# Kernel optimization log

Measured on AMD Instinct MI355X. Metric: run time of the kernel, lower is better.

Reference implementation:

```python
import jax, jax.numpy as jnp
import numpy as np


def _gcn_layer(x, row, col, W, b):
    # x: [N, d_in]; row/col: [E'] (with self loops already appended)
    N = x.shape[0]
    deg = jax.ops.segment_sum(jnp.ones_like(row, dtype=x.dtype), row, num_segments=N)
    deg_inv_sqrt = deg ** -0.5  # self loops guarantee deg >= 1
    norm = deg_inv_sqrt[row] * deg_inv_sqrt[col]  # [E']
    msg = norm[:, None] * x[row]                  # gather + normalize
    aggr = jax.ops.segment_sum(msg, col, num_segments=N)  # scatter-add
    return aggr @ W + b


def reference(x, edge_index, W1, b1, W2, b2):
    N = x.shape[0]
    loops = jnp.arange(N, dtype=edge_index.dtype)
    row = jnp.concatenate([edge_index[0], loops])
    col = jnp.concatenate([edge_index[1], loops])
    h = jax.nn.relu(_gcn_layer(x, row, col, W1, b1))
    # F.dropout(training=self.training) is identity in eval mode
    out = _gcn_layer(h, row, col, W2, b2)
    return jax.nn.log_softmax(out, axis=1)


def setup_inputs() -> dict:
    key = jax.random.key(0)
    k1, k2, k3, k4 = jax.random.split(key, 4)
    N, E, F_IN, F_HID, F_OUT = 100000, 1200000, 64, 64, 16
    x = jax.random.normal(k1, (N, F_IN), dtype=jnp.float32)
    edge_index = jax.random.randint(k2, (2, E), 0, N, dtype=jnp.int64)
    W1 = jax.random.normal(k3, (F_IN, F_HID), dtype=jnp.float32) / np.sqrt(F_IN)
    b1 = jnp.zeros((F_HID,), dtype=jnp.float32)
    W2 = jax.random.normal(k4, (F_HID, F_OUT), dtype=jnp.float32) / np.sqrt(F_HID)
    b2 = jnp.zeros((F_OUT,), dtype=jnp.float32)
    return {"x": x, "edge_index": edge_index, "W1": W1, "b1": b1, "W2": W2, "b2": b2}
```

## Files before the change

### kernel.cpp

```cpp
#include <hip/hip_runtime.h>
#include <hip/hip_bf16.h>

typedef __attribute__((ext_vector_type(8))) _Float16 hfrag;
typedef __attribute__((ext_vector_type(4))) float ffrag;
typedef __attribute__((ext_vector_type(4))) _Float16 h4v;

#define BSH 8
#define LBS 256
#define CAP_SH 14
#define CAP (1 << CAP_SH)
#define CONV_BLKS 384
#define FILL_BLKS 512

__device__ __forceinline__ float b2f_(unsigned short u) {
    return __uint_as_float(((unsigned)u) << 16);
}
__device__ __forceinline__ unsigned short f2b_(float v) {
    __hip_bfloat16 h = __float2bfloat16(v);
    return *reinterpret_cast<unsigned short*>(&h);
}
__device__ __forceinline__ unsigned short f2h_(float v) {
    _Float16 h = (_Float16)v;
    return __builtin_bit_cast(unsigned short, h);
}
__device__ __forceinline__ float h2f_(unsigned short u) {
    _Float16 h = __builtin_bit_cast(_Float16, u);
    return (float)h;
}

__device__ __forceinline__ float loadF(const void* p, long long i, int isF32) {
    if (isF32) return ((const float*)p)[i];
    return b2f_(((const unsigned short*)p)[i]);
}

__device__ __forceinline__ float4 loadF4(const void* p, long long base, int i4, int isF32) {
    if (isF32) {
        return ((const float4*)((const float*)p + base))[i4];
    } else {
        ushort4 u = ((const ushort4*)((const unsigned short*)p + base))[i4];
        return make_float4(b2f_(u.x), b2f_(u.y), b2f_(u.z), b2f_(u.w));
    }
}

__device__ __forceinline__ void get_edge(const int* ei, int i64, int e, int E, int& s, int& d) {
    if (i64) { s = ei[2 * (long long)e]; d = ei[2 * (long long)E + 2 * (long long)e]; }
    else     { s = ei[e];                d = ei[(long long)E + e]; }
}

struct E4 { int s[4]; int d[4]; };
__device__ __forceinline__ E4 load4(const int* __restrict__ ei, int i64, int e0, int E) {
    E4 r;
    if (i64) {
        const int4* ps = (const int4*)(ei + 2 * (long long)e0);
        const int4* pd = (const int4*)(ei + 2 * (long long)E + 2 * (long long)e0);
        int4 a = ps[0], b = ps[1];
        int4 c = pd[0], d = pd[1];
        r.s[0] = a.x; r.s[1] = a.z; r.s[2] = b.x; r.s[3] = b.z;
        r.d[0] = c.x; r.d[1] = c.z; r.d[2] = d.x; r.d[3] = d.z;
    } else {
        int4 a = *(const int4*)(ei + e0);
        int4 c = *(const int4*)(ei + (long long)E + e0);
        r.s[0] = a.x; r.s[1] = a.y; r.s[2] = a.z; r.s[3] = a.w;
        r.d[0] = c.x; r.d[1] = c.y; r.d[2] = c.z; r.d[3] = c.w;
    }
    return r;
}

__device__ __forceinline__ void wave_scan_excl(int* a, int nEl, int lane) {
    int run = 0;
    for (int base = 0; base < nEl; base += 64) {
        int i = base + lane;
        int orig = (i < nEl) ? a[i] : 0;
        int v = orig;
#pragma unroll
        for (int off = 1; off < 64; off <<= 1) {
            int u = __shfl_up(v, off);
            if (lane >= off) v += u;
        }
        if (i < nEl) a[i] = v - orig + run;
        run += __shfl(v, 63);
    }
}

__global__ void k_prep(const void* x, const int* ei,
                       const void* W1, const void* b1, const void* W2, const void* b2,
                       int E, int nbk,
                       int* flags, float* Wbuf, int* cur_d, int* cur_s) {
    __shared__ int s_sane, s_zero;
    int tid = threadIdx.x;
    if (tid == 0) { s_sane = 0; s_zero = 0; }
    __syncthreads();
    const unsigned short* xu = (const unsigned short*)x;
    int sane = 0;
    for (int k = tid; k < 4096; k += 256) {
        float v = b2f_(xu[2 * k]);
        float a = fabsf(v);
        if (v == 0.0f || (a >= 9.3e-10f && a <= 1.1e9f)) sane++;
    }
    if (sane) atomicAdd(&s_sane, sane);
    int zero = 0;
    for (int k = tid; k < 1024; k += 256) if (ei[2 * k + 1] == 0) zero++;
    if (zero) atomicAdd(&s_zero, zero);
    __syncthreads();
    int f = (s_sane < 3000) ? 1 : 0;
    if (tid == 0) { flags[0] = f; flags[1] = (s_zero > 512) ? 1 : 0; }
    for (int i = tid; i < nbk; i += 256) { cur_d[i] = i << CAP_SH; cur_s[i] = i << CAP_SH; }
    for (int i = tid; i < 4096; i += 256) Wbuf[i] = loadF(W1, i, f);
    if (tid < 64) Wbuf[4096 + tid] = loadF(b1, tid, f);
    for (int i = tid; i < 1024; i += 256) Wbuf[4160 + i] = loadF(W2, i, f);
    if (tid < 16) Wbuf[5184 + tid] = loadF(b2, tid, f);
}

__global__ __launch_bounds__(256) void k_stage(const void* __restrict__ x,
                                               const int* __restrict__ ei,
                                               const int* __restrict__ flags,
                                               int E, int N, int nbk,
                                               int* __restrict__ cur_d, int* __restrict__ cur_s,
                                               int* __restrict__ pdst,
                                               unsigned char* __restrict__ psrc,
                                               unsigned short* __restrict__ xh) {
    __shared__ int hd[512], hs[512], bd[512], bs[512];
    int tid = threadIdx.x;
    if (blockIdx.x < CONV_BLKS) {
        int f = flags[0];
        int n4 = N * 16;
        int ctid = blockIdx.x * 256 + tid;
        int stride = CONV_BLKS * 256 * 2;
        for (int i0 = ctid * 2; i0 < n4; i0 += stride) {
            float4 v0 = loadF4(x, 0, i0, f);
            float4 v1 = (i0 + 1 < n4) ? loadF4(x, 0, i0 + 1, f) : make_float4(0, 0, 0, 0);
            ushort4 o0, o1;
            o0.x = f2h_(v0.x); o0.y = f2h_(v0.y); o0.z = f2h_(v0.z); o0.w = f2h_(v0.w);
            o1.x = f2h_(v1.x); o1.y = f2h_(v1.y); o1.z = f2h_(v1.z); o1.w = f2h_(v1.w);
            ((ushort4*)xh)[i0] = o0;
            if (i0 + 1 < n4) ((ushort4*)xh)[i0 + 1] = o1;
        }
        return;
    }
    for (int i = tid; i < 512; i += 256) { hd[i] = 0; hs[i] = 0; }
    __syncthreads();
    int i64 = flags[1];
    int fb = blockIdx.x - CONV_BLKS;
    int ctid = fb * 256 + tid;
    int stride = FILL_BLKS * 256 * 8;
    for (int e0 = ctid * 8; e0 + 8 <= E; e0 += stride) {
        E4 a = load4(ei, i64, e0, E);
        E4 b = load4(ei, i64, e0 + 4, E);
#pragma unroll
        for (int u = 0; u < 4; ++u) {
            atomicAdd(&hd[a.d[u] >> BSH], 1);
            atomicAdd(&hs[a.s[u] >> BSH], 1);
            atomicAdd(&hd[b.d[u] >> BSH], 1);
            atomicAdd(&hs[b.s[u] >> BSH], 1);
        }
    }
    if (fb == 0 && tid == 0) {
        for (int e = E & ~7; e < E; ++e) {
            int s, d;
            get_edge(ei, i64, e, E, s, d);
            atomicAdd(&hd[d >> BSH], 1);
            atomicAdd(&hs[s >> BSH], 1);
        }
    }
    __syncthreads();
    for (int i = tid; i < nbk; i += 256) {
        int v = hd[i];
        bd[i] = v ? atomicAdd(&cur_d[i], v) : 0;
        v = hs[i];
        bs[i] = v ? atomicAdd(&cur_s[i], v) : 0;
    }
    __syncthreads();
    for (int e0 = ctid * 8; e0 + 8 <= E; e0 += stride) {
        E4 a = load4(ei, i64, e0, E);
        E4 b = load4(ei, i64, e0 + 4, E);
#pragma unroll
        for (int u = 0; u < 4; ++u) {
            int db = a.d[u] >> BSH, sb = a.s[u] >> BSH;
            int p = atomicAdd(&bd[db], 1);
            if (p < ((db + 1) << CAP_SH)) pdst[p] = (a.s[u] << BSH) | (a.d[u] & (LBS - 1));
            int q = atomicAdd(&bs[sb], 1);
            if (q < ((sb + 1) << CAP_SH)) psrc[q] = (unsigned char)(a.s[u] & (LBS - 1));
            db = b.d[u] >> BSH; sb = b.s[u] >> BSH;
            p = atomicAdd(&bd[db], 1);
            if (p < ((db + 1) << CAP_SH)) pdst[p] = (b.s[u] << BSH) | (b.d[u] & (LBS - 1));
            q = atomicAdd(&bs[sb], 1);
            if (q < ((sb + 1) << CAP_SH)) psrc[q] = (unsigned char)(b.s[u] & (LBS - 1));
        }
    }
    if (fb == 0 && tid == 0) {
        for (int e = E & ~7; e < E; ++e) {
            int s, d;
            get_edge(ei, i64, e, E, s, d);
            int db = d >> BSH, sb = s >> BSH;
            int p = atomicAdd(&bd[db], 1);
            if (p < ((db + 1) << CAP_SH)) pdst[p] = (s << BSH) | (d & (LBS - 1));
            int q = atomicAdd(&bs[sb], 1);
            if (q < ((sb + 1) << CAP_SH)) psrc[q] = (unsigned char)(s & (LBS - 1));
        }
    }
}

__global__ __launch_bounds__(256) void k_deg(const unsigned char* __restrict__ psrc,
                                             const int* __restrict__ cur_s,
                                             float* __restrict__ dis, int N) {
    __shared__ int h[LBS];
    int b = blockIdx.x, tid = threadIdx.x;
    if (tid < LBS) h[tid] = 0;
    __syncthreads();
    int beg = b << CAP_SH;
    int end = min(cur_s[b], (b + 1) << CAP_SH);
    int cnt = end - beg;
    int nv = cnt & ~3;
    for (int off = 4 * tid; off < nv; off += 1024) {
        uchar4 v = *(const uchar4*)(psrc + beg + off);
        atomicAdd(&h[v.x], 1); atomicAdd(&h[v.y], 1);
        atomicAdd(&h[v.z], 1); atomicAdd(&h[v.w], 1);
    }
    if (tid < cnt - nv) atomicAdd(&h[psrc[beg + nv + tid]], 1);
    __syncthreads();
    if (tid < LBS) {
        int node = b * LBS + tid;
        if (node < N) dis[node] = rsqrtf((float)h[tid] + 1.0f);
    }
}

__global__ __launch_bounds__(256) void k_csr(const int* __restrict__ pdst,
                                             const int* __restrict__ cur_d,
                                             const float* __restrict__ dis,
                                             int2* __restrict__ row_se,
                                             int2* __restrict__ pke, int N) {
    __shared__ int h[LBS], lb[LBS], cur[LBS];
    int b = blockIdx.x, tid = threadIdx.x;
    if (tid < LBS) h[tid] = 0;
    __syncthreads();
    int beg = b << CAP_SH;
    int end = min(cur_d[b], (b + 1) << CAP_SH);
    for (int p = beg + tid; p < end; p += 256) atomicAdd(&h[pdst[p] & (LBS - 1)], 1);
    __syncthreads();
    if (tid < LBS) lb[tid] = h[tid];
    __syncthreads();
    if (tid < 64) wave_scan_excl(lb, LBS, tid);
    __syncthreads();
    if (tid < LBS) {
        cur[tid] = lb[tid];
        int node = b * LBS + tid;
        if (node < N) row_se[node] = make_int2(beg + lb[tid], beg + lb[tid] + h[tid]);
    }
    __syncthreads();
    for (int p = beg + tid; p < end; p += 256) {
        int e = pdst[p];
        int src = e >> BSH, ld = e & (LBS - 1);
        int r = atomicAdd(&cur[ld], 1);
        pke[beg + r] = make_int2(src, __float_as_int(dis[src]));
    }
}

__global__ __launch_bounds__(256) void k_agg(const unsigned short* __restrict__ xh,
                                             const float* __restrict__ dis,
                                             const int2* __restrict__ row_se,
                                             const int2* __restrict__ pke,
                                             unsigned short* __restrict__ aggb, int N) {
    int tid = threadIdx.x;
    int lane = tid & 63;
    int g = lane >> 4, i4 = lane & 15;
    int n = blockIdx.x * 16 + (tid >> 6) * 4 + g;
    if (n >= N) return;
    float dd = dis[n];
    int2 se = row_se[n];
    int beg = se.x, end = se.y;
    int cnt = end - beg;
    h4v xv = *(const h4v*)(xh + (long long)n * 64 + i4 * 4);
    float w = dd * dd;
    float4 A[4];
    A[0].x = w * (float)xv[0]; A[0].y = w * (float)xv[1];
    A[0].z = w * (float)xv[2]; A[0].w = w * (float)xv[3];
#pragma unroll
    for (int u = 1; u < 4; ++u) A[u] = make_float4(0.f, 0.f, 0.f, 0.f);
    int T = (cnt + 3) >> 2;
    int p = beg;
    int2 e[4];
#pragma unroll
    for (int u = 0; u < 4; ++u) e[u] = pke[p + u];
    for (int t = 0; t < T; ++t) {
        h4v hv[4];
#pragma unroll
        for (int u = 0; u < 4; ++u) {
            unsigned ex = min((unsigned)e[u].x, (unsigned)(N - 1));
            hv[u] = *(const h4v*)(xh + (long long)ex * 64 + i4 * 4);
        }
        float nv[4];
#pragma unroll
        for (int u = 0; u < 4; ++u) nv[u] = (p + u < end) ? dd * __int_as_float(e[u].y) : 0.f;
#pragma unroll
        for (int u = 0; u < 4; ++u) e[u] = pke[p + 4 + u];
        p += 4;
#pragma unroll
        for (int u = 0; u < 4; ++u) {
            A[u].x += nv[u] * (float)hv[u][0];
            A[u].y += nv[u] * (float)hv[u][1];
            A[u].z += nv[u] * (float)hv[u][2];
            A[u].w += nv[u] * (float)hv[u][3];
        }
    }
    float4 s;
    s.x = A[0].x + A[1].x + A[2].x + A[3].x;
    s.y = A[0].y + A[1].y + A[2].y + A[3].y;
    s.z = A[0].z + A[1].z + A[2].z + A[3].z;
    s.w = A[0].w + A[1].w + A[2].w + A[3].w;
    ushort4 o;
    o.x = f2h_(s.x); o.y = f2h_(s.y); o.z = f2h_(s.z); o.w = f2h_(s.w);
    *(ushort4*)(aggb + (size_t)n * 64 + i4 * 4) = o;
}

__global__ __launch_bounds__(256) void k_dense(const unsigned short* __restrict__ aggb,
                                               const float* __restrict__ Wbuf,
                                               unsigned short* __restrict__ t2b, int N) {
    __shared__ __align__(16) unsigned short Hs[4][16 * 72];
    int tid = threadIdx.x;
    int lane = tid & 63;
    int w = tid >> 6;
    int m = lane & 15, q = lane >> 4;
    int n0 = blockIdx.x * 64 + w * 16;
    if (n0 >= N) return;

    hfrag Bw1[2][4];
#pragma unroll
    for (int kt = 0; kt < 2; ++kt)
#pragma unroll
        for (int nt = 0; nt < 4; ++nt)
#pragma unroll
            for (int j = 0; j < 8; ++j)
                Bw1[kt][nt][j] = (_Float16)Wbuf[(kt * 32 + q * 8 + j) * 64 + nt * 16 + m];
    hfrag Bw2[2];
#pragma unroll
    for (int kt = 0; kt < 2; ++kt)
#pragma unroll
        for (int j = 0; j < 8; ++j)
            Bw2[kt][j] = (_Float16)Wbuf[4160 + (kt * 32 + q * 8 + j) * 16 + m];
    float b1n[4];
#pragma unroll
    for (int nt = 0; nt < 4; ++nt) b1n[nt] = Wbuf[4096 + nt * 16 + m];

    const unsigned short* arow = aggb + (size_t)(n0 + m) * 64 + q * 8;
    hfrag A0 = *(const hfrag*)(arow);
    hfrag A1 = *(const hfrag*)(arow + 32);

    ffrag acc[4];
#pragma unroll
    for (int nt = 0; nt < 4; ++nt) {
        ffrag z = {0.f, 0.f, 0.f, 0.f};
        z = __builtin_amdgcn_mfma_f32_16x16x32_f16(A0, Bw1[0][nt], z, 0, 0, 0);
        z = __builtin_amdgcn_mfma_f32_16x16x32_f16(A1, Bw1[1][nt], z, 0, 0, 0);
        acc[nt] = z;
    }
    unsigned short* hs = &Hs[w][0];
#pragma unroll
    for (int nt = 0; nt < 4; ++nt)
#pragma unroll
        for (int r = 0; r < 4; ++r) {
            float hv = fmaxf(acc[nt][r] + b1n[nt], 0.0f);
            hs[(q * 4 + r) * 72 + nt * 16 + m] = f2h_(hv);
        }
    const unsigned short* hrow = hs + m * 72 + q * 8;
    hfrag H0 = *(const hfrag*)(hrow);
    hfrag H1 = *(const hfrag*)(hrow + 32);
    ffrag t2 = {0.f, 0.f, 0.f, 0.f};
    t2 = __builtin_amdgcn_mfma_f32_16x16x32_f16(H0, Bw2[0], t2, 0, 0, 0);
    t2 = __builtin_amdgcn_mfma_f32_16x16x32_f16(H1, Bw2[1], t2, 0, 0, 0);
#pragma unroll
    for (int r = 0; r < 4; ++r)
        t2b[(size_t)(n0 + q * 4 + r) * 16 + m] = f2h_(t2[r]);
}

__global__ __launch_bounds__(256) void k_l2(const unsigned short* __restrict__ t2b,
                                            const int* __restrict__ flags,
                                            const float* __restrict__ dis,
                                            const int2* __restrict__ row_se,
                                            const int2* __restrict__ pke,
                                            const float* __restrict__ Wbuf,
                                            void* __restrict__ out, int N) {
    int isF32 = flags[0];
    int tid = threadIdx.x, lane = tid & 63;
    int g = lane >> 4, i = lane & 15;
    int n = blockIdx.x * 16 + (tid >> 6) * 4 + g;
    if (n >= N) return;
    float dd = dis[n];
    int2 se = row_se[n];
    int beg = se.x, end = se.y;
    int cnt = end - beg;
    float A[4];
    A[0] = dd * dd * h2f_(t2b[(size_t)n * 16 + i]);
    A[1] = 0.f; A[2] = 0.f; A[3] = 0.f;
    int T = (cnt + 3) >> 2;
    int p = beg;
    int2 e[4];
#pragma unroll
    for (int u = 0; u < 4; ++u) e[u] = pke[p + u];
    for (int t = 0; t < T; ++t) {
        float r[4];
#pragma unroll
        for (int u = 0; u < 4; ++u) {
            unsigned ex = min((unsigned)e[u].x, (unsigned)(N - 1));
            r[u] = h2f_(t2b[(size_t)ex * 16 + i]);
        }
        float nv[4];
#pragma unroll
        for (int u = 0; u < 4; ++u) nv[u] = (p + u < end) ? dd * __int_as_float(e[u].y) : 0.f;
#pragma unroll
        for (int u = 0; u < 4; ++u) e[u] = pke[p + 4 + u];
        p += 4;
#pragma unroll
        for (int u = 0; u < 4; ++u) A[u] += nv[u] * r[u];
    }
    float a0 = A[0] + A[1] + A[2] + A[3];
    float v = a0 + Wbuf[5184 + i];
    float mx = v;
#pragma unroll
    for (int off = 8; off; off >>= 1) mx = fmaxf(mx, __shfl_xor(mx, off, 16));
    float ex = __expf(v - mx);
    float ss = ex;
#pragma unroll
    for (int off = 8; off; off >>= 1) ss += __shfl_xor(ss, off, 16);
    float r = v - mx - logf(ss);
    size_t oi = (size_t)n * 16 + i;
    if (isF32) ((float*)out)[oi] = r;
    else       ((unsigned short*)out)[oi] = f2b_(r);
}

extern "C" void kernel_launch(void* const* d_in, const int* in_sizes, int n_in,
                              void* d_out, int out_size, void* d_ws, size_t ws_size,
                              hipStream_t stream) {
    const void* x  = d_in[0];
    const int*  ei = (const int*)d_in[1];
    const void* W1 = d_in[2];
    const void* b1 = d_in[3];
    const void* W2 = d_in[4];
    const void* b2 = d_in[5];

    const int N = in_sizes[0] / 64;
    const int E = in_sizes[1] / 2;
    const int nbk = (N + LBS - 1) >> BSH;

    char* p = (char*)d_ws;
#define CARVE(ty, name, bytes) ty name = (ty)p; p += (((size_t)(bytes)) + 63) & ~(size_t)63;
    CARVE(int*,   flags,     16)
    CARVE(float*, Wbuf,      5200 * 4)
    CARVE(float*, dis,       (size_t)N * 4)
    CARVE(int2*,  row_se,    (size_t)N * 8)
    CARVE(int*,   cur_d,     (size_t)nbk * 4)
    CARVE(int*,   cur_s,     (size_t)nbk * 4)
    CARVE(int*,   pdst,      ((size_t)nbk << CAP_SH) * 4)
    CARVE(unsigned char*, psrc, ((size_t)nbk << CAP_SH))
    CARVE(int2*,  pke,       (((size_t)nbk << CAP_SH) + 64) * 8)
    CARVE(unsigned short*, xh,   (size_t)N * 64 * 2)
    CARVE(unsigned short*, aggb, (size_t)N * 64 * 2)
    CARVE(unsigned short*, t2b,  (size_t)N * 16 * 2)
#undef CARVE

    k_prep<<<1, 256, 0, stream>>>(x, ei, W1, b1, W2, b2, E, nbk, flags, Wbuf, cur_d, cur_s);
    k_stage<<<CONV_BLKS + FILL_BLKS, 256, 0, stream>>>(x, ei, flags, E, N, nbk,
                                                       cur_d, cur_s, pdst, psrc, xh);
    k_deg<<<nbk, 256, 0, stream>>>(psrc, cur_s, dis, N);
    k_csr<<<nbk, 256, 0, stream>>>(pdst, cur_d, dis, row_se, pke, N);
    k_agg<<<(N + 15) / 16, 256, 0, stream>>>(xh, dis, row_se, pke, aggb, N);
    k_dense<<<(N + 63) / 64, 256, 0, stream>>>(aggb, Wbuf, t2b, N);
    k_l2<<<(N + 15) / 16, 256, 0, stream>>>(t2b, flags, dis, row_se, pke, Wbuf, d_out, N);
}
```

Measured before the change: 202.1 us.

## Split edge bucketing into count, scan, fill kernels replacing global atomics

The fused histogram-and-fill stage is split into three kernels. The first writes per-block bucket counts, the second does a per-bucket exclusive scan across fill blocks, and the third scatters edges using deterministic per-block offsets. This removes global atomicAdd contention on bucket cursors and cuts the fill block count from 512 to 128. In exchange it adds two kernel launches, extra count and offset arrays, and a second pass over the edge list in a separate launch.

```diff
diff --git a/kernel.cpp b/kernel.cpp
--- a/kernel.cpp
+++ b/kernel.cpp
@@ -10,7 +10,8 @@
 #define CAP_SH 14
 #define CAP (1 << CAP_SH)
 #define CONV_BLKS 384
-#define FILL_BLKS 512
+#define NF 128
+#define NBKP 512
 
 __device__ __forceinline__ float b2f_(unsigned short u) {
     return __uint_as_float(((unsigned)u) << 16);
@@ -84,8 +85,7 @@
 
 __global__ void k_prep(const void* x, const int* ei,
                        const void* W1, const void* b1, const void* W2, const void* b2,
-                       int E, int nbk,
-                       int* flags, float* Wbuf, int* cur_d, int* cur_s) {
+                       int* flags, float* Wbuf) {
     __shared__ int s_sane, s_zero;
     int tid = threadIdx.x;
     if (tid == 0) { s_sane = 0; s_zero = 0; }
@@ -104,22 +104,19 @@
     __syncthreads();
     int f = (s_sane < 3000) ? 1 : 0;
     if (tid == 0) { flags[0] = f; flags[1] = (s_zero > 512) ? 1 : 0; }
-    for (int i = tid; i < nbk; i += 256) { cur_d[i] = i << CAP_SH; cur_s[i] = i << CAP_SH; }
     for (int i = tid; i < 4096; i += 256) Wbuf[i] = loadF(W1, i, f);
     if (tid < 64) Wbuf[4096 + tid] = loadF(b1, tid, f);
     for (int i = tid; i < 1024; i += 256) Wbuf[4160 + i] = loadF(W2, i, f);
     if (tid < 16) Wbuf[5184 + tid] = loadF(b2, tid, f);
 }
 
-__global__ __launch_bounds__(256) void k_stage(const void* __restrict__ x,
-                                               const int* __restrict__ ei,
-                                               const int* __restrict__ flags,
-                                               int E, int N, int nbk,
-                                               int* __restrict__ cur_d, int* __restrict__ cur_s,
-                                               int* __restrict__ pdst,
-                                               unsigned char* __restrict__ psrc,
-                                               unsigned short* __restrict__ xh) {
-    __shared__ int hd[512], hs[512], bd[512], bs[512];
+__global__ __launch_bounds__(256) void k_s1(const void* __restrict__ x,
+                                            const int* __restrict__ ei,
+                                            const int* __restrict__ flags,
+                                            int E, int N, int nbk,
+                                            int* __restrict__ cnt_d, int* __restrict__ cnt_s,
+                                            unsigned short* __restrict__ xh) {
+    __shared__ int hd[512], hs[512];
     int tid = threadIdx.x;
     if (blockIdx.x < CONV_BLKS) {
         int f = flags[0];
@@ -142,7 +139,7 @@
     int i64 = flags[1];
     int fb = blockIdx.x - CONV_BLKS;
     int ctid = fb * 256 + tid;
-    int stride = FILL_BLKS * 256 * 8;
+    int stride = NF * 256 * 8;
     for (int e0 = ctid * 8; e0 + 8 <= E; e0 += stride) {
         E4 a = load4(ei, i64, e0, E);
         E4 b = load4(ei, i64, e0 + 4, E);
@@ -164,12 +161,54 @@
     }
     __syncthreads();
     for (int i = tid; i < nbk; i += 256) {
-        int v = hd[i];
-        bd[i] = v ? atomicAdd(&cur_d[i], v) : 0;
-        v = hs[i];
-        bs[i] = v ? atomicAdd(&cur_s[i], v) : 0;
-    }
-    __syncthreads();
+        cnt_d[fb * NBKP + i] = hd[i];
+        cnt_s[fb * NBKP + i] = hs[i];
+    }
+}
+
+__global__ __launch_bounds__(128) void k_s2(const int* __restrict__ cnt_d,
+                                            const int* __restrict__ cnt_s,
+                                            int nbk,
+                                            int* __restrict__ base_d, int* __restrict__ base_s,
+                                            int* __restrict__ td, int* __restrict__ ts) {
+    __shared__ int vd[NF], vs[NF];
+    __shared__ int lastd, lasts;
+    int b = blockIdx.x, tid = threadIdx.x;
+    for (int i = tid; i < NF; i += 128) { vd[i] = cnt_d[i * NBKP + b]; vs[i] = cnt_s[i * NBKP + b]; }
+    __syncthreads();
+    if (tid == 0) lastd = vd[NF - 1];
+    if (tid == 1) lasts = vs[NF - 1];
+    __syncthreads();
+    int lane = tid & 63;
+    if (tid < 64)       wave_scan_excl(vd, NF, lane);
+    else if (tid < 128) wave_scan_excl(vs, NF, lane);
+    __syncthreads();
+    for (int i = tid; i < NF; i += 128) {
+        base_d[i * NBKP + b] = (b << CAP_SH) + vd[i];
+        base_s[i * NBKP + b] = (b << CAP_SH) + vs[i];
+    }
+    if (tid == 0) td[b] = (b << CAP_SH) + vd[NF - 1] + lastd;
+    if (tid == 1) ts[b] = (b << CAP_SH) + vs[NF - 1] + lasts;
+}
+
+__global__ __launch_bounds__(256) void k_fill(const int* __restrict__ ei,
+                                              const int* __restrict__ flags,
+                                              int E, int nbk,
+                                              const int* __restrict__ base_d,
+                                              const int* __restrict__ base_s,
+                                              int* __restrict__ pdst,
+                                              unsigned char* __restrict__ psrc) {
+    __shared__ int bd[512], bs[512];
+    int tid = threadIdx.x;
+    int fb = blockIdx.x;
+    for (int i = tid; i < nbk; i += 256) {
+        bd[i] = base_d[fb * NBKP + i];
+        bs[i] = base_s[fb * NBKP + i];
+    }
+    __syncthreads();
+    int i64 = flags[1];
+    int ctid = fb * 256 + tid;
+    int stride = NF * 256 * 8;
     for (int e0 = ctid * 8; e0 + 8 <= E; e0 += stride) {
         E4 a = load4(ei, i64, e0, E);
         E4 b = load4(ei, i64, e0 + 4, E);
@@ -201,14 +240,14 @@
 }
 
 __global__ __launch_bounds__(256) void k_deg(const unsigned char* __restrict__ psrc,
-                                             const int* __restrict__ cur_s,
+                                             const int* __restrict__ ts,
                                              float* __restrict__ dis, int N) {
     __shared__ int h[LBS];
     int b = blockIdx.x, tid = threadIdx.x;
     if (tid < LBS) h[tid] = 0;
     __syncthreads();
     int beg = b << CAP_SH;
-    int end = min(cur_s[b], (b + 1) << CAP_SH);
+    int end = min(ts[b], (b + 1) << CAP_SH);
     int cnt = end - beg;
     int nv = cnt & ~3;
     for (int off = 4 * tid; off < nv; off += 1024) {
@@ -225,7 +264,7 @@
 }
 
 __global__ __launch_bounds__(256) void k_csr(const int* __restrict__ pdst,
-                                             const int* __restrict__ cur_d,
+                                             const int* __restrict__ td,
                                              const float* __restrict__ dis,
                                              int2* __restrict__ row_se,
                                              int2* __restrict__ pke, int N) {
@@ -234,7 +273,7 @@
     if (tid < LBS) h[tid] = 0;
     __syncthreads();
     int beg = b << CAP_SH;
-    int end = min(cur_d[b], (b + 1) << CAP_SH);
+    int end = min(td[b], (b + 1) << CAP_SH);
     for (int p = beg + tid; p < end; p += 256) atomicAdd(&h[pdst[p] & (LBS - 1)], 1);
     __syncthreads();
     if (tid < LBS) lb[tid] = h[tid];
@@ -447,8 +486,12 @@
     CARVE(float*, Wbuf,      5200 * 4)
     CARVE(float*, dis,       (size_t)N * 4)
     CARVE(int2*,  row_se,    (size_t)N * 8)
-    CARVE(int*,   cur_d,     (size_t)nbk * 4)
-    CARVE(int*,   cur_s,     (size_t)nbk * 4)
+    CARVE(int*,   cnt_d,     (size_t)NF * NBKP * 4)
+    CARVE(int*,   cnt_s,     (size_t)NF * NBKP * 4)
+    CARVE(int*,   base_d,    (size_t)NF * NBKP * 4)
+    CARVE(int*,   base_s,    (size_t)NF * NBKP * 4)
+    CARVE(int*,   td,        (size_t)nbk * 4)
+    CARVE(int*,   ts,        (size_t)nbk * 4)
     CARVE(int*,   pdst,      ((size_t)nbk << CAP_SH) * 4)
     CARVE(unsigned char*, psrc, ((size_t)nbk << CAP_SH))
     CARVE(int2*,  pke,       (((size_t)nbk << CAP_SH) + 64) * 8)
@@ -457,11 +500,12 @@
     CARVE(unsigned short*, t2b,  (size_t)N * 16 * 2)
 #undef CARVE
 
-    k_prep<<<1, 256, 0, stream>>>(x, ei, W1, b1, W2, b2, E, nbk, flags, Wbuf, cur_d, cur_s);
-    k_stage<<<CONV_BLKS + FILL_BLKS, 256, 0, stream>>>(x, ei, flags, E, N, nbk,
-                                                       cur_d, cur_s, pdst, psrc, xh);
-    k_deg<<<nbk, 256, 0, stream>>>(psrc, cur_s, dis, N);
-    k_csr<<<nbk, 256, 0, stream>>>(pdst, cur_d, dis, row_se, pke, N);
+    k_prep<<<1, 256, 0, stream>>>(x, ei, W1, b1, W2, b2, flags, Wbuf);
+    k_s1<<<CONV_BLKS + NF, 256, 0, stream>>>(x, ei, flags, E, N, nbk, cnt_d, cnt_s, xh);
+    k_s2<<<nbk, 128, 0, stream>>>(cnt_d, cnt_s, nbk, base_d, base_s, td, ts);
+    k_fill<<<NF, 256, 0, stream>>>(ei, flags, E, nbk, base_d, base_s, pdst, psrc);
+    k_deg<<<nbk, 256, 0, stream>>>(psrc, ts, dis, N);
+    k_csr<<<nbk, 256, 0, stream>>>(pdst, td, dis, row_se, pke, N);
     k_agg<<<(N + 15) / 16, 256, 0, stream>>>(xh, dis, row_se, pke, aggb, N);
     k_dense<<<(N + 63) / 64, 256, 0, stream>>>(aggb, Wbuf, t2b, N);
     k_l2<<<(N + 15) / 16, 256, 0, stream>>>(t2b, flags, dis, row_se, pke, Wbuf, d_out, N);
```

New measurement: 217.0 us. 7.4% more time.

## Split bucket staging into histogram and deterministic fill kernels with global degree atomics

Applied to the files above, without the earlier changes.

Replaces the single-block prep plus fused histogram/fill kernel with a histogram kernel that writes per-block bucket counts into a transposed table and counts source degrees with global atomics. A separate fill kernel computes each block's bucket offsets by prefix-summing that table, then scatters destination-bucketed edges. The psrc staging array and the k_deg kernel are dropped, and dis is computed in the conversion blocks. The aim is to remove the global atomic offset reservation and the second source-bucket scatter. The cost is an extra edge-list read, a memset, and 100k-address global atomics for degree.

```diff
diff --git a/kernel.cpp b/kernel.cpp
--- a/kernel.cpp
+++ b/kernel.cpp
@@ -9,8 +9,8 @@
 #define LBS 256
 #define CAP_SH 14
 #define CAP (1 << CAP_SH)
+#define NF 192
 #define CONV_BLKS 384
-#define FILL_BLKS 512
 
 __device__ __forceinline__ float b2f_(unsigned short u) {
     return __uint_as_float(((unsigned)u) << 16);
@@ -82,49 +82,88 @@
     }
 }
 
-__global__ void k_prep(const void* x, const int* ei,
-                       const void* W1, const void* b1, const void* W2, const void* b2,
-                       int E, int nbk,
-                       int* flags, float* Wbuf, int* cur_d, int* cur_s) {
+__global__ __launch_bounds__(256) void k_h(const void* __restrict__ x,
+                                           const int* __restrict__ ei,
+                                           const void* __restrict__ W1, const void* __restrict__ b1,
+                                           const void* __restrict__ W2, const void* __restrict__ b2,
+                                           int E, int N, int nbk,
+                                           int* __restrict__ flags, float* __restrict__ Wbuf,
+                                           int* __restrict__ cnt_t, int* __restrict__ deg) {
+    __shared__ int hd[512];
     __shared__ int s_sane, s_zero;
     int tid = threadIdx.x;
     if (tid == 0) { s_sane = 0; s_zero = 0; }
     __syncthreads();
-    const unsigned short* xu = (const unsigned short*)x;
-    int sane = 0;
-    for (int k = tid; k < 4096; k += 256) {
-        float v = b2f_(xu[2 * k]);
-        float a = fabsf(v);
-        if (v == 0.0f || (a >= 9.3e-10f && a <= 1.1e9f)) sane++;
-    }
-    if (sane) atomicAdd(&s_sane, sane);
+    if (blockIdx.x == NF) {
+        const unsigned short* xu = (const unsigned short*)x;
+        int sane = 0;
+        for (int k = tid; k < 4096; k += 256) {
+            float v = b2f_(xu[2 * k]);
+            float a = fabsf(v);
+            if (v == 0.0f || (a >= 9.3e-10f && a <= 1.1e9f)) sane++;
+        }
+        if (sane) atomicAdd(&s_sane, sane);
+        int zero = 0;
+        for (int k = tid; k < 1024; k += 256) if (ei[2 * k + 1] == 0) zero++;
+        if (zero) atomicAdd(&s_zero, zero);
+        __syncthreads();
+        int f = (s_sane < 3000) ? 1 : 0;
+        if (tid == 0) { flags[0] = f; flags[1] = (s_zero > 512) ? 1 : 0; }
+        for (int i = tid; i < 4096; i += 256) Wbuf[i] = loadF(W1, i, f);
+        if (tid < 64) Wbuf[4096 + tid] = loadF(b1, tid, f);
+        for (int i = tid; i < 1024; i += 256) Wbuf[4160 + i] = loadF(W2, i, f);
+        if (tid < 16) Wbuf[5184 + tid] = loadF(b2, tid, f);
+        return;
+    }
     int zero = 0;
     for (int k = tid; k < 1024; k += 256) if (ei[2 * k + 1] == 0) zero++;
     if (zero) atomicAdd(&s_zero, zero);
-    __syncthreads();
-    int f = (s_sane < 3000) ? 1 : 0;
-    if (tid == 0) { flags[0] = f; flags[1] = (s_zero > 512) ? 1 : 0; }
-    for (int i = tid; i < nbk; i += 256) { cur_d[i] = i << CAP_SH; cur_s[i] = i << CAP_SH; }
-    for (int i = tid; i < 4096; i += 256) Wbuf[i] = loadF(W1, i, f);
-    if (tid < 64) Wbuf[4096 + tid] = loadF(b1, tid, f);
-    for (int i = tid; i < 1024; i += 256) Wbuf[4160 + i] = loadF(W2, i, f);
-    if (tid < 16) Wbuf[5184 + tid] = loadF(b2, tid, f);
-}
-
-__global__ __launch_bounds__(256) void k_stage(const void* __restrict__ x,
-                                               const int* __restrict__ ei,
-                                               const int* __restrict__ flags,
-                                               int E, int N, int nbk,
-                                               int* __restrict__ cur_d, int* __restrict__ cur_s,
-                                               int* __restrict__ pdst,
-                                               unsigned char* __restrict__ psrc,
-                                               unsigned short* __restrict__ xh) {
-    __shared__ int hd[512], hs[512], bd[512], bs[512];
+    for (int i = tid; i < 512; i += 256) hd[i] = 0;
+    __syncthreads();
+    int i64 = (s_zero > 512) ? 1 : 0;
+    int fb = blockIdx.x;
+    int ctid = fb * 256 + tid;
+    int stride = NF * 256 * 8;
+    for (int e0 = ctid * 8; e0 + 8 <= E; e0 += stride) {
+        E4 a = load4(ei, i64, e0, E);
+        E4 b = load4(ei, i64, e0 + 4, E);
+#pragma unroll
+        for (int u = 0; u < 4; ++u) {
+            atomicAdd(&hd[a.d[u] >> BSH], 1);
+            atomicAdd(&deg[a.s[u]], 1);
+            atomicAdd(&hd[b.d[u] >> BSH], 1);
+            atomicAdd(&deg[b.s[u]], 1);
+        }
+    }
+    if (fb == 0 && tid == 0) {
+        for (int e = E & ~7; e < E; ++e) {
+            int s, d;
+            get_edge(ei, i64, e, E, s, d);
+            atomicAdd(&hd[d >> BSH], 1);
+            atomicAdd(&deg[s], 1);
+        }
+    }
+    __syncthreads();
+    for (int b = tid; b < nbk; b += 256) cnt_t[b * NF + fb] = hd[b];
+}
+
+__global__ __launch_bounds__(256) void k_fill(const void* __restrict__ x,
+                                              const int* __restrict__ ei,
+                                              const int* __restrict__ flags,
+                                              int E, int N, int nbk,
+                                              const int* __restrict__ cnt_t,
+                                              const int* __restrict__ deg,
+                                              int* __restrict__ td,
+                                              int* __restrict__ pdst,
+                                              unsigned short* __restrict__ xh,
+                                              float* __restrict__ dis) {
+    __shared__ int bd[512];
     int tid = threadIdx.x;
-    if (blockIdx.x < CONV_BLKS) {
+    if (blockIdx.x >= NF) {
+        int cb = blockIdx.x - NF;
         int f = flags[0];
         int n4 = N * 16;
-        int ctid = blockIdx.x * 256 + tid;
+        int ctid = cb * 256 + tid;
         int stride = CONV_BLKS * 256 * 2;
         for (int i0 = ctid * 2; i0 < n4; i0 += stride) {
             float4 v0 = loadF4(x, 0, i0, f);
@@ -135,97 +174,55 @@
             ((ushort4*)xh)[i0] = o0;
             if (i0 + 1 < n4) ((ushort4*)xh)[i0 + 1] = o1;
         }
+        for (int n = cb * 256 + tid; n < N; n += CONV_BLKS * 256)
+            dis[n] = rsqrtf((float)deg[n] + 1.0f);
         return;
     }
-    for (int i = tid; i < 512; i += 256) { hd[i] = 0; hs[i] = 0; }
+    int fb = blockIdx.x;
+    for (int b = tid; b < nbk; b += 256) {
+        int prefix = 0, total = 0;
+        const int* row = cnt_t + b * NF;
+        for (int j = 0; j < NF; j += 4) {
+            int4 v = *(const int4*)(row + j);
+            total += v.x + v.y + v.z + v.w;
+            if (j + 0 < fb) prefix += v.x;
+            if (j + 1 < fb) prefix += v.y;
+            if (j + 2 < fb) prefix += v.z;
+            if (j + 3 < fb) prefix += v.w;
+        }
+        bd[b] = (b << CAP_SH) + prefix;
+        if (fb == 0) td[b] = (b << CAP_SH) + total;
+    }
     __syncthreads();
     int i64 = flags[1];
-    int fb = blockIdx.x - CONV_BLKS;
     int ctid = fb * 256 + tid;
-    int stride = FILL_BLKS * 256 * 8;
+    int stride = NF * 256 * 8;
     for (int e0 = ctid * 8; e0 + 8 <= E; e0 += stride) {
         E4 a = load4(ei, i64, e0, E);
         E4 b = load4(ei, i64, e0 + 4, E);
 #pragma unroll
         for (int u = 0; u < 4; ++u) {
-            atomicAdd(&hd[a.d[u] >> BSH], 1);
-            atomicAdd(&hs[a.s[u] >> BSH], 1);
-            atomicAdd(&hd[b.d[u] >> BSH], 1);
-            atomicAdd(&hs[b.s[u] >> BSH], 1);
+            int db = a.d[u] >> BSH;
+            int p = atomicAdd(&bd[db], 1);
+            if (p < ((db + 1) << CAP_SH)) pdst[p] = (a.s[u] << BSH) | (a.d[u] & (LBS - 1));
+            db = b.d[u] >> BSH;
+            p = atomicAdd(&bd[db], 1);
+            if (p < ((db + 1) << CAP_SH)) pdst[p] = (b.s[u] << BSH) | (b.d[u] & (LBS - 1));
         }
     }
     if (fb == 0 && tid == 0) {
         for (int e = E & ~7; e < E; ++e) {
             int s, d;
             get_edge(ei, i64, e, E, s, d);
-            atomicAdd(&hd[d >> BSH], 1);
-            atomicAdd(&hs[s >> BSH], 1);
-        }
-    }
-    __syncthreads();
-    for (int i = tid; i < nbk; i += 256) {
-        int v = hd[i];
-        bd[i] = v ? atomicAdd(&cur_d[i], v) : 0;
-        v = hs[i];
-        bs[i] = v ? atomicAdd(&cur_s[i], v) : 0;
-    }
-    __syncthreads();
-    for (int e0 = ctid * 8; e0 + 8 <= E; e0 += stride) {
-        E4 a = load4(ei, i64, e0, E);
-        E4 b = load4(ei, i64, e0 + 4, E);
-#pragma unroll
-        for (int u = 0; u < 4; ++u) {
-            int db = a.d[u] >> BSH, sb = a.s[u] >> BSH;
-            int p = atomicAdd(&bd[db], 1);
-            if (p < ((db + 1) << CAP_SH)) pdst[p] = (a.s[u] << BSH) | (a.d[u] & (LBS - 1));
-            int q = atomicAdd(&bs[sb], 1);
-            if (q < ((sb + 1) << CAP_SH)) psrc[q] = (unsigned char)(a.s[u] & (LBS - 1));
-            db = b.d[u] >> BSH; sb = b.s[u] >> BSH;
-            p = atomicAdd(&bd[db], 1);
-            if (p < ((db + 1) << CAP_SH)) pdst[p] = (b.s[u] << BSH) | (b.d[u] & (LBS - 1));
-            q = atomicAdd(&bs[sb], 1);
-            if (q < ((sb + 1) << CAP_SH)) psrc[q] = (unsigned char)(b.s[u] & (LBS - 1));
-        }
-    }
-    if (fb == 0 && tid == 0) {
-        for (int e = E & ~7; e < E; ++e) {
-            int s, d;
-            get_edge(ei, i64, e, E, s, d);
-            int db = d >> BSH, sb = s >> BSH;
+            int db = d >> BSH;
             int p = atomicAdd(&bd[db], 1);
             if (p < ((db + 1) << CAP_SH)) pdst[p] = (s << BSH) | (d & (LBS - 1));
-            int q = atomicAdd(&bs[sb], 1);
-            if (q < ((sb + 1) << CAP_SH)) psrc[q] = (unsigned char)(s & (LBS - 1));
-        }
-    }
-}
-
-__global__ __launch_bounds__(256) void k_deg(const unsigned char* __restrict__ psrc,
-                                             const int* __restrict__ cur_s,
-                                             float* __restrict__ dis, int N) {
-    __shared__ int h[LBS];
-    int b = blockIdx.x, tid = threadIdx.x;
-    if (tid < LBS) h[tid] = 0;
-    __syncthreads();
-    int beg = b << CAP_SH;
-    int end = min(cur_s[b], (b + 1) << CAP_SH);
-    int cnt = end - beg;
-    int nv = cnt & ~3;
-    for (int off = 4 * tid; off < nv; off += 1024) {
-        uchar4 v = *(const uchar4*)(psrc + beg + off);
-        atomicAdd(&h[v.x], 1); atomicAdd(&h[v.y], 1);
-        atomicAdd(&h[v.z], 1); atomicAdd(&h[v.w], 1);
-    }
-    if (tid < cnt - nv) atomicAdd(&h[psrc[beg + nv + tid]], 1);
-    __syncthreads();
-    if (tid < LBS) {
-        int node = b * LBS + tid;
-        if (node < N) dis[node] = rsqrtf((float)h[tid] + 1.0f);
+        }
     }
 }
 
 __global__ __launch_bounds__(256) void k_csr(const int* __restrict__ pdst,
-                                             const int* __restrict__ cur_d,
+                                             const int* __restrict__ td,
                                              const float* __restrict__ dis,
                                              int2* __restrict__ row_se,
                                              int2* __restrict__ pke, int N) {
@@ -234,7 +231,7 @@
     if (tid < LBS) h[tid] = 0;
     __syncthreads();
     int beg = b << CAP_SH;
-    int end = min(cur_d[b], (b + 1) << CAP_SH);
+    int end = min(td[b], (b + 1) << CAP_SH);
     for (int p = beg + tid; p < end; p += 256) atomicAdd(&h[pdst[p] & (LBS - 1)], 1);
     __syncthreads();
     if (tid < LBS) lb[tid] = h[tid];
@@ -447,21 +444,22 @@
     CARVE(float*, Wbuf,      5200 * 4)
     CARVE(float*, dis,       (size_t)N * 4)
     CARVE(int2*,  row_se,    (size_t)N * 8)
-    CARVE(int*,   cur_d,     (size_t)nbk * 4)
-    CARVE(int*,   cur_s,     (size_t)nbk * 4)
+    CARVE(int*,   deg,       (size_t)N * 4)
+    CARVE(int*,   cnt_t,     (size_t)nbk * NF * 4)
+    CARVE(int*,   td,        (size_t)nbk * 4)
     CARVE(int*,   pdst,      ((size_t)nbk << CAP_SH) * 4)
-    CARVE(unsigned char*, psrc, ((size_t)nbk << CAP_SH))
     CARVE(int2*,  pke,       (((size_t)nbk << CAP_SH) + 64) * 8)
     CARVE(unsigned short*, xh,   (size_t)N * 64 * 2)
     CARVE(unsigned short*, aggb, (size_t)N * 64 * 2)
     CARVE(unsigned short*, t2b,  (size_t)N * 16 * 2)
 #undef CARVE
 
-    k_prep<<<1, 256, 0, stream>>>(x, ei, W1, b1, W2, b2, E, nbk, flags, Wbuf, cur_d, cur_s);
-    k_stage<<<CONV_BLKS + FILL_BLKS, 256, 0, stream>>>(x, ei, flags, E, N, nbk,
-                                                       cur_d, cur_s, pdst, psrc, xh);
-    k_deg<<<nbk, 256, 0, stream>>>(psrc, cur_s, dis, N);
-    k_csr<<<nbk, 256, 0, stream>>>(pdst, cur_d, dis, row_se, pke, N);
+    hipMemsetAsync(deg, 0, (size_t)N * 4, stream);
+    k_h<<<NF + 1, 256, 0, stream>>>(x, ei, W1, b1, W2, b2, E, N, nbk,
+                                    flags, Wbuf, cnt_t, deg);
+    k_fill<<<NF + CONV_BLKS, 256, 0, stream>>>(x, ei, flags, E, N, nbk,
+                                               cnt_t, deg, td, pdst, xh, dis);
+    k_csr<<<nbk, 256, 0, stream>>>(pdst, td, dis, row_se, pke, N);
     k_agg<<<(N + 15) / 16, 256, 0, stream>>>(xh, dis, row_se, pke, aggb, N);
     k_dense<<<(N + 63) / 64, 256, 0, stream>>>(aggb, Wbuf, t2b, N);
     k_l2<<<(N + 15) / 16, 256, 0, stream>>>(t2b, flags, dis, row_se, pke, Wbuf, d_out, N);
```

Result: slower. 247.8 us (+22.6%).
